# Kernel optimization log

Hardware: AMD Instinct MI355X
Metric: run time of the kernel (lower is better)

Reference implementation:

```python
import jax, jax.numpy as jnp
import numpy as np

V, E, D, T, B = 32000, 512, 512, 512, 32
PAD = 3

def layer_norm(x, g, b, eps=1e-5):
    m = jnp.mean(x, axis=-1, keepdims=True)
    v = jnp.mean((x - m) ** 2, axis=-1, keepdims=True)
    return (x - m) * jax.lax.rsqrt(v + eps) * g + b

def sru_direction(U, v, b, reverse):
    # U: (T, B, 4D) -> splits: x_tilde, f-gate pre-act, r-gate pre-act, highway input
    x_t, uf, ur, xp = jnp.split(U, 4, axis=-1)
    def step(c, inp):
        xt, uft, urt, xpt = inp
        f = jax.nn.sigmoid(uft + v[0] * c + b[0])
        r = jax.nn.sigmoid(urt + v[1] * c + b[1])
        c_new = f * c + (1.0 - f) * xt
        h = r * c_new + (1.0 - r) * xpt
        return c_new, h
    c0 = jnp.zeros((U.shape[1], v.shape[1]), U.dtype)  # (B, D)
    c_last, hs = jax.lax.scan(step, c0, (x_t, uf, ur, xp), reverse=reverse)
    return hs, c_last

def setup_inputs() -> dict:
    key = jax.random.key(0)
    ks = jax.random.split(key, 8)
    def rn(k, shp, sc=0.05):
        return jax.random.normal(k, shp, jnp.float32) * sc
    return {
        "src": jax.random.randint(ks[0], (T, B), 0, V),
        "emb": rn(ks[1], (V, E), 0.1),
        "ln_g": jnp.ones((E,), jnp.float32),
        "ln_b": jnp.zeros((E,), jnp.float32),
        "W0": rn(ks[2], (E, 4 * D)),
        "W1": rn(ks[3], (E, 4 * D)),
        "v0": rn(ks[4], (2, D), 0.5),
        "v1": rn(ks[5], (2, D), 0.5),
        "b0": jnp.zeros((2, D), jnp.float32),
        "b1": jnp.zeros((2, D), jnp.float32),
        "W_out": rn(ks[6], (D, 2 * D)),
        "b_out": jnp.zeros((D,), jnp.float32),
    }

def reference(src, emb, ln_g, ln_b, W0, W1, v0, v1, b0, b1, W_out, b_out):
    table = emb.at[PAD].set(0.0)          # padding_idx row is zero
    x = table[src]                         # (T, B, E); dropout p=0 -> identity
    xn = layer_norm(x, ln_g, ln_b)         # SRU layer_norm=True: LN on cell input
    h0, c0 = sru_direction(jnp.einsum('tbe,ef->tbf', xn, W0), v0, b0, False)
    h1, c1 = sru_direction(jnp.einsum('tbe,ef->tbf', xn, W1), v1, b1, True)
    outputs = jnp.concatenate([h0, h1], axis=-1)        # (T, B, 2D)
    hidden = jnp.concatenate([c0, c1], axis=-1)[None]   # (1, B, 2D)
    out = jnp.tanh(jnp.einsum('tbh,dh->tbd', outputs, W_out) + b_out)
    return out, hidden
```

## Files before the change

### kernel.cpp

```cpp
#include <hip/hip_runtime.h>
#include <cstdint>
#include <cstddef>

#define T_DIM 512
#define B_DIM 32
#define E_DIM 512
#define D_DIM 512
#define PAD_IDX 3
#define M_ROWS (T_DIM * B_DIM)
#define PF 32

typedef __attribute__((ext_vector_type(8))) __bf16 bf16x8;
typedef __attribute__((ext_vector_type(4))) float  f32x4;

__device__ __forceinline__ unsigned short f2bf(float x) {
    union { float f; uint32_t u; } v; v.f = x;
    uint32_t u = v.u;
    uint32_t r = (u + 0x7FFFu + ((u >> 16) & 1u)) >> 16;
    return (unsigned short)r;
}
__device__ __forceinline__ float bf2f(unsigned short h) {
    union { float f; uint32_t u; } v; v.u = ((uint32_t)h) << 16;
    return v.f;
}
__device__ __forceinline__ float fast_sigmoid(float z) {
    return __builtin_amdgcn_rcpf(1.f + __expf(-z));
}
__device__ __forceinline__ float fast_tanh(float x) {
    return 1.f - 2.f * __builtin_amdgcn_rcpf(__expf(2.f * x) + 1.f);
}

__global__ __launch_bounds__(256) void prep_kernel(
    const int* __restrict__ src, const float* __restrict__ emb,
    const float* __restrict__ g, const float* __restrict__ bb,
    const float* __restrict__ W0, const float* __restrict__ W1,
    const float* __restrict__ b0, const float* __restrict__ b1,
    const float* __restrict__ W_out,
    unsigned short* __restrict__ xn, unsigned short* __restrict__ Wt,
    unsigned short* __restrict__ Wob, float* __restrict__ bias)
{
    __shared__ float tile[64][65];
    const int bx = blockIdx.x;
    if (bx < 4096) {
        int wave = threadIdx.x >> 6;
        int lane = threadIdx.x & 63;
        int row  = bx * 4 + wave;
        int tok  = src[row];
        float x[8];
        if (tok == PAD_IDX) {
            #pragma unroll
            for (int j = 0; j < 8; j++) x[j] = 0.f;
        } else {
            const float* er = emb + (size_t)tok * E_DIM + lane * 8;
            f32x4 a0 = *(const f32x4*)(er);
            f32x4 a1 = *(const f32x4*)(er + 4);
            #pragma unroll
            for (int j = 0; j < 4; j++) { x[j] = a0[j]; x[4 + j] = a1[j]; }
        }
        float s = 0.f, sq = 0.f;
        #pragma unroll
        for (int j = 0; j < 8; j++) { s += x[j]; sq += x[j] * x[j]; }
        #pragma unroll
        for (int off = 32; off >= 1; off >>= 1) {
            s  += __shfl_xor(s,  off, 64);
            sq += __shfl_xor(sq, off, 64);
        }
        float mean = s * (1.f / 512.f);
        float var  = sq * (1.f / 512.f) - mean * mean;
        float rs   = rsqrtf(var + 1e-5f);
        f32x4 g0 = *(const f32x4*)(g + lane * 8);
        f32x4 g1 = *(const f32x4*)(g + lane * 8 + 4);
        f32x4 c0 = *(const f32x4*)(bb + lane * 8);
        f32x4 c1 = *(const f32x4*)(bb + lane * 8 + 4);
        unsigned short o[8];
        #pragma unroll
        for (int j = 0; j < 4; j++) {
            o[j]     = f2bf((x[j]     - mean) * rs * g0[j] + c0[j]);
            o[4 + j] = f2bf((x[4 + j] - mean) * rs * g1[j] + c1[j]);
        }
        uint4 pk;
        pk.x = (uint32_t)o[0] | ((uint32_t)o[1] << 16);
        pk.y = (uint32_t)o[2] | ((uint32_t)o[3] << 16);
        pk.z = (uint32_t)o[4] | ((uint32_t)o[5] << 16);
        pk.w = (uint32_t)o[6] | ((uint32_t)o[7] << 16);
        *(uint4*)(xn + (size_t)row * E_DIM + lane * 8) = pk;
    } else if (bx < 4608) {
        int bxx = bx - 4096;
        int k0  = (bxx & 7) * 64;
        int n0g = (bxx >> 3) * 64;
        int dir = n0g >> 11;
        const float* W = dir ? W1 : W0;
        int d0 = (n0g & 2047) >> 2;
        int tx = threadIdx.x & 63;
        int ty = threadIdx.x >> 6;
        int scol = ((tx >> 4) << 9) + d0 + (tx & 15);
        for (int r = ty; r < 64; r += 4)
            tile[r][tx] = W[(size_t)(k0 + r) * 2048 + scol];
        __syncthreads();
        for (int r2 = ty; r2 < 64; r2 += 4) {
            int j = ((r2 & 3) << 4) | (r2 >> 2);
            Wt[(size_t)(n0g + r2) * 512 + k0 + tx] = f2bf(tile[tx][j]);
        }
    } else if (bx < 5120) {
        int i = ((bx - 4608) * 256 + threadIdx.x) * 4;
        f32x4 v = *(const f32x4*)(W_out + i);
        uint2 pk;
        pk.x = (uint32_t)f2bf(v[0]) | ((uint32_t)f2bf(v[1]) << 16);
        pk.y = (uint32_t)f2bf(v[2]) | ((uint32_t)f2bf(v[3]) << 16);
        *(uint2*)(Wob + i) = pk;
    } else {
        int n = (bx - 5120) * 256 + threadIdx.x;
        int dir = n >> 11, gg = n & 3, d = (n & 2047) >> 2;
        const float* bp = dir ? b1 : b0;
        float v = (gg == 1) ? bp[d] : ((gg == 2) ? bp[512 + d] : 0.f);
        bias[n] = v;
    }
}

template<int KD, int NMT, int NNT, int GM, int GN, int EPI>
__global__ __launch_bounds__(512, 4) void gemm_pipe_kernel(
    const unsigned short* __restrict__ A,
    const unsigned short* __restrict__ Bt,
    void* __restrict__ Cout,
    const float* __restrict__ bias,
    int ldc)
{
    constexpr int BM = 128, BN = 256;
    constexpr int MR = 4, NR = 4;
    constexpr int NKT = KD / 32;
    constexpr int RA  = BM / 128;
    constexpr int RB  = BN / 128;
    constexpr int LPT = RA + RB;
    constexpr int ASZ = BM * 32;
    constexpr int BSZ = BN * 32;
    __shared__ unsigned short smem[3 * (ASZ + BSZ)];

    const int tid = threadIdx.x;
    const int w   = tid >> 6;
    const int l   = tid & 63;

    constexpr int PER_G = GM * GN;
    constexpr int NGC   = NNT / GN;
    const int bid = blockIdx.x;
    const int c   = bid & 7;
    const int idx = bid >> 3;
    const int gi  = idx / PER_G;
    const int wi  = idx % PER_G;
    const int gg  = c + 8 * gi;
    const int mt  = (gg / NGC) * GM + wi / GN;
    const int nt  = (gg % NGC) * GN + wi % GN;

    const int wm = w >> 2, wn = w & 3;

    const unsigned short* Ab = A  + (size_t)mt * BM * KD;
    const unsigned short* Bb = Bt + (size_t)nt * BN * KD;

    const int srow = w * 16 + (l >> 2);
    const int scol = ((l & 3) ^ ((l >> 3) & 3)) * 8;

    auto stage = [&](int t, int slot) {
        const unsigned short* Ag = Ab + t * 32;
        const unsigned short* Bg = Bb + t * 32;
        unsigned short* As = smem + slot * (ASZ + BSZ);
        unsigned short* Bs = As + ASZ;
        #pragma unroll
        for (int r = 0; r < RA; r++)
            __builtin_amdgcn_global_load_lds(
                (const __attribute__((address_space(1))) void*)(Ag + (size_t)(r * 128 + srow) * KD + scol),
                (__attribute__((address_space(3))) void*)(As + (r * 128 + w * 16) * 32),
                16, 0, 0);
        #pragma unroll
        for (int r = 0; r < RB; r++)
            __builtin_amdgcn_global_load_lds(
                (const __attribute__((address_space(1))) void*)(Bg + (size_t)(r * 128 + srow) * KD + scol),
                (__attribute__((address_space(3))) void*)(Bs + (r * 128 + w * 16) * 32),
                16, 0, 0);
    };

    f32x4 acc[MR][NR];
    #pragma unroll
    for (int m = 0; m < MR; m++)
        #pragma unroll
        for (int n = 0; n < NR; n++)
            acc[m][n] = (f32x4){0.f, 0.f, 0.f, 0.f};

    stage(0, 0); stage(1, 1);

    const int li   = l & 15;
    const int cg   = l >> 4;
    const int rswz = (cg ^ ((li >> 1) & 3)) * 8;

    #pragma unroll
    for (int t = 0; t < NKT; t++) {
        if (t + 1 < NKT)
            asm volatile("s_waitcnt vmcnt(%0) lgkmcnt(0)" :: "n"(LPT) : "memory");
        else
            asm volatile("s_waitcnt vmcnt(0) lgkmcnt(0)" ::: "memory");
        __builtin_amdgcn_s_barrier();
        if (t + 2 < NKT) stage(t + 2, (t + 2) % 3);

        const unsigned short* As = smem + (t % 3) * (ASZ + BSZ);
        const unsigned short* Bs = As + ASZ;
        bf16x8 af[MR], bfv[NR];
        #pragma unroll
        for (int m = 0; m < MR; m++) {
            int row = wm * 64 + m * 16 + li;
            af[m] = *(const bf16x8*)(As + row * 32 + rswz);
        }
        #pragma unroll
        for (int n = 0; n < NR; n++) {
            int row = wn * 64 + n * 16 + li;
            bfv[n] = *(const bf16x8*)(Bs + row * 32 + rswz);
        }
        __builtin_amdgcn_s_setprio(1);
        #pragma unroll
        for (int m = 0; m < MR; m++)
            #pragma unroll
            for (int n = 0; n < NR; n++)
                acc[m][n] = __builtin_amdgcn_mfma_f32_16x16x32_bf16(
                    af[m], bfv[n], acc[m][n], 0, 0, 0);
        __builtin_amdgcn_s_setprio(0);
    }

    const int colb = nt * BN + wn * 64;
    const int rowb = mt * BM + wm * 64;
    #pragma unroll
    for (int m = 0; m < MR; m++) {
        #pragma unroll
        for (int n = 0; n < NR; n++) {
            int col  = colb + n * 16 + li;
            int row0 = rowb + m * 16 + cg * 4;
            float bi = bias[col];
            if (EPI == 0) {
                unsigned short* C = (unsigned short*)Cout;
                #pragma unroll
                for (int j = 0; j < 4; j++)
                    C[(size_t)(row0 + j) * ldc + col] = f2bf(acc[m][n][j] + bi);
            } else {
                float* C = (float*)Cout;
                #pragma unroll
                for (int j = 0; j < 4; j++)
                    C[(size_t)(row0 + j) * ldc + col] = fast_tanh(acc[m][n][j] + bi);
            }
        }
    }
}

template<int KD, int NMT, int NNT, int GM, int GN, int EPI>
__global__ __launch_bounds__(256, 3) void gemm_ring3_kernel(
    const unsigned short* __restrict__ A,
    const unsigned short* __restrict__ Bt,
    void* __restrict__ Cout,
    const float* __restrict__ bias,
    int ldc)
{
    constexpr int NKT = KD / 32;
    constexpr int LPT = 4;
    constexpr int SLOT = 8192;
    __shared__ unsigned short smem[3 * SLOT];

    const int tid = threadIdx.x;
    const int w   = tid >> 6;
    const int l   = tid & 63;

    constexpr int PER_G = GM * GN;
    constexpr int NGC   = NNT / GN;
    const int bid = blockIdx.x;
    const int c   = bid & 7;
    const int idx = bid >> 3;
    const int gi  = idx / PER_G;
    const int wi  = idx % PER_G;
    const int gg  = c + 8 * gi;
    const int mt  = (gg / NGC) * GM + wi / GN;
    const int nt  = (gg % NGC) * GN + wi % GN;

    const int wm = w >> 1, wn = w & 1;

    const unsigned short* Ab = A  + (size_t)mt * 128 * KD;
    const unsigned short* Bb = Bt + (size_t)nt * 128 * KD;

    const int s_colx = (((l & 3) ^ ((l >> 3) & 3)) * 8);

    auto stage = [&](int t, int slot) {
        const unsigned short* Ag = Ab + t * 32 + s_colx;
        const unsigned short* Bg = Bb + t * 32 + s_colx;
        unsigned short* As = smem + slot * SLOT;
        unsigned short* Bs = As + 4096;
        #pragma unroll
        for (int r = 0; r < 2; r++) {
            int grow = r * 64 + w * 16 + (l >> 2);
            __builtin_amdgcn_global_load_lds(
                (const __attribute__((address_space(1))) void*)(Ag + (size_t)grow * KD),
                (__attribute__((address_space(3))) void*)(As + r * 2048 + w * 512),
                16, 0, 0);
            __builtin_amdgcn_global_load_lds(
                (const __attribute__((address_space(1))) void*)(Bg + (size_t)grow * KD),
                (__attribute__((address_space(3))) void*)(Bs + r * 2048 + w * 512),
                16, 0, 0);
        }
    };

    f32x4 acc[4][4];
    #pragma unroll
    for (int m = 0; m < 4; m++)
        #pragma unroll
        for (int n = 0; n < 4; n++)
            acc[m][n] = (f32x4){0.f, 0.f, 0.f, 0.f};

    stage(0, 0); stage(1, 1);

    const int li   = l & 15;
    const int cg   = l >> 4;
    const int rswz = (cg ^ ((li >> 1) & 3)) * 8;

    #pragma unroll
    for (int t = 0; t < NKT; t++) {
        if (t + 1 < NKT)
            asm volatile("s_waitcnt vmcnt(%0) lgkmcnt(0)" :: "n"(LPT) : "memory");
        else
            asm volatile("s_waitcnt vmcnt(0) lgkmcnt(0)" ::: "memory");
        __builtin_amdgcn_s_barrier();
        if (t + 2 < NKT) stage(t + 2, (t + 2) % 3);

        const unsigned short* As = smem + (t % 3) * SLOT;
        const unsigned short* Bs = As + 4096;
        bf16x8 af[4], bfv[4];
        #pragma unroll
        for (int m = 0; m < 4; m++) {
            int row = wm * 64 + m * 16 + li;
            af[m] = *(const bf16x8*)(As + row * 32 + rswz);
        }
        #pragma unroll
        for (int n = 0; n < 4; n++) {
            int row = wn * 64 + n * 16 + li;
            bfv[n] = *(const bf16x8*)(Bs + row * 32 + rswz);
        }
        __builtin_amdgcn_s_setprio(1);
        #pragma unroll
        for (int m = 0; m < 4; m++)
            #pragma unroll
            for (int n = 0; n < 4; n++)
                acc[m][n] = __builtin_amdgcn_mfma_f32_16x16x32_bf16(
                    af[m], bfv[n], acc[m][n], 0, 0, 0);
        __builtin_amdgcn_s_setprio(0);
    }

    const int colb = nt * 128 + wn * 64;
    const int rowb = mt * 128 + wm * 64;
    #pragma unroll
    for (int m = 0; m < 4; m++) {
        #pragma unroll
        for (int n = 0; n < 4; n++) {
            int col  = colb + n * 16 + li;
            int row0 = rowb + m * 16 + cg * 4;
            float bi = bias[col];
            if (EPI == 0) {
                unsigned short* C = (unsigned short*)Cout;
                #pragma unroll
                for (int j = 0; j < 4; j++)
                    C[(size_t)(row0 + j) * ldc + col] = f2bf(acc[m][n][j] + bi);
            } else {
                float* C = (float*)Cout;
                #pragma unroll
                for (int j = 0; j < 4; j++)
                    C[(size_t)(row0 + j) * ldc + col] = fast_tanh(acc[m][n][j] + bi);
            }
        }
    }
}

__global__ __launch_bounds__(64) void sru_scan_kernel(
    const unsigned short* __restrict__ U,
    const float* __restrict__ v0, const float* __restrict__ v1,
    unsigned short* __restrict__ h,
    float* __restrict__ hidden)
{
    int id  = blockIdx.x * 64 + threadIdx.x;
    int dir = id >> 14;
    int rem = id & 16383;
    int b   = rem >> 9;
    int d   = rem & 511;
    const float* v = dir ? v1 : v0;
    float vf = v[d], vr = v[D_DIM + d];

    int row0  = (dir ? (T_DIM - 1) * B_DIM : 0) + b;
    long step = (long)(dir ? -B_DIM : B_DIM) * 1024;

    const ushort4* lp = (const ushort4*)U + (size_t)row0 * 1024 + dir * 512 + d;
    unsigned short* hp = h + (size_t)row0 * 1024 + dir * 512 + d;

    ushort4 buf[PF];
    #pragma unroll
    for (int p = 0; p < PF; p++) { buf[p] = *lp; lp += step; }

    float c = 0.f;
    for (int tb = 0; tb < T_DIM - PF; tb += PF) {
        #pragma unroll
        for (int p = 0; p < PF; p++) {
            ushort4 q = buf[p];
            buf[p] = *lp; lp += step;
            float x  = bf2f(q.x);
            float uf = bf2f(q.y);
            float ur = bf2f(q.z);
            float xp = bf2f(q.w);
            float f = fast_sigmoid(__fmaf_rn(vf, c, uf));
            float r = fast_sigmoid(__fmaf_rn(vr, c, ur));
            c = __fmaf_rn(f, c - x, x);
            float hv = __fmaf_rn(r, c - xp, xp);
            *hp = f2bf(hv); hp += step;
        }
    }
    #pragma unroll
    for (int p = 0; p < PF; p++) {
        ushort4 q = buf[p];
        float x  = bf2f(q.x);
        float uf = bf2f(q.y);
        float ur = bf2f(q.z);
        float xp = bf2f(q.w);
        float f = fast_sigmoid(__fmaf_rn(vf, c, uf));
        float r = fast_sigmoid(__fmaf_rn(vr, c, ur));
        c = __fmaf_rn(f, c - x, x);
        float hv = __fmaf_rn(r, c - xp, xp);
        *hp = f2bf(hv); hp += step;
    }
    hidden[b * 1024 + dir * 512 + d] = c;
}

extern "C" void kernel_launch(void* const* d_in, const int* in_sizes, int n_in,
                              void* d_out, int out_size, void* d_ws, size_t ws_size,
                              hipStream_t stream)
{
    const int*   src   = (const int*)  d_in[0];
    const float* emb   = (const float*)d_in[1];
    const float* ln_g  = (const float*)d_in[2];
    const float* ln_b  = (const float*)d_in[3];
    const float* W0    = (const float*)d_in[4];
    const float* W1    = (const float*)d_in[5];
    const float* v0    = (const float*)d_in[6];
    const float* v1    = (const float*)d_in[7];
    const float* b0    = (const float*)d_in[8];
    const float* b1    = (const float*)d_in[9];
    const float* W_out = (const float*)d_in[10];
    const float* b_out = (const float*)d_in[11];

    unsigned short* Wt  = (unsigned short*)d_ws;
    unsigned short* Wob = Wt  + (size_t)4096 * 512;
    unsigned short* xn  = Wob + (size_t)512 * 1024;
    unsigned short* U   = xn  + (size_t)M_ROWS * 512;
    unsigned short* h   = U   + (size_t)M_ROWS * 4096;
    float*          bias4096 = (float*)(h + (size_t)M_ROWS * 1024);

    float* out    = (float*)d_out;
    float* hidden = out + (size_t)M_ROWS * D_DIM;
    (void)out;

    prep_kernel<<<5136, 256, 0, stream>>>(src, emb, ln_g, ln_b, W0, W1,
                                          b0, b1, W_out, xn, Wt, Wob, bias4096);

    gemm_pipe_kernel<512, 128, 16, 8, 4, 0>
        <<<2048, 512, 0, stream>>>(xn, Wt, (void*)U, bias4096, 4096);

    sru_scan_kernel<<<512, 64, 0, stream>>>(U, v0, v1, h, hidden);

    gemm_ring3_kernel<1024, 128, 4, 8, 2, 1>
        <<<512, 256, 0, stream>>>(h, Wob, (void*)d_out, b_out, 512);
}
```

Measured before the change: 154.1 us.

## Load B operand straight into registers for the input GEMM and reuse pipe kernel for output GEMM

Adds a GEMM variant for the large U projection in which each wave loads its B (weight) fragments directly from global memory into a double-buffered register array. Only the A tile is staged through LDS with a three-slot ring. This shrinks LDS use and the B-side LDS traffic, at the cost of more VGPRs and uncoalesced 16-byte global loads. The output projection switches from the 256-thread ring3 kernel to the 512-thread, 128x256-tile pipe kernel with 256 blocks, and the ring3 kernel is removed.

```diff
diff --git a/kernel.cpp b/kernel.cpp
--- a/kernel.cpp
+++ b/kernel.cpp
@@ -117,6 +117,118 @@
     }
 }
 
+template<int KD, int NMT, int NNT, int GM, int GN>
+__global__ __launch_bounds__(512, 4) void gemm_breg_kernel(
+    const unsigned short* __restrict__ A,
+    const unsigned short* __restrict__ Bt,
+    unsigned short* __restrict__ C,
+    const float* __restrict__ bias,
+    int ldc)
+{
+    constexpr int NKT = KD / 32;
+    constexpr int ASZ = 128 * 32;
+    __shared__ unsigned short smem[3 * ASZ];
+
+    const int tid = threadIdx.x;
+    const int w   = tid >> 6;
+    const int l   = tid & 63;
+
+    constexpr int PER_G = GM * GN;
+    constexpr int NGC   = NNT / GN;
+    const int bid = blockIdx.x;
+    const int c   = bid & 7;
+    const int idx = bid >> 3;
+    const int gi  = idx / PER_G;
+    const int wi  = idx % PER_G;
+    const int gg  = c + 8 * gi;
+    const int mt  = (gg / NGC) * GM + wi / GN;
+    const int nt  = (gg % NGC) * GN + wi % GN;
+
+    const int wm = w >> 2, wn = w & 3;
+    const int li = l & 15;
+    const int cg = l >> 4;
+
+    const unsigned short* Ab = A + (size_t)mt * 128 * KD;
+    const unsigned short* bp = Bt + (size_t)(nt * 256 + wn * 64 + li) * KD + cg * 8;
+
+    const int srow = w * 16 + (l >> 2);
+    const int scol = ((l & 3) ^ ((l >> 3) & 3)) * 8;
+
+    auto stageA = [&](int t, int slot) {
+        __builtin_amdgcn_global_load_lds(
+            (const __attribute__((address_space(1))) void*)(Ab + (size_t)srow * KD + t * 32 + scol),
+            (__attribute__((address_space(3))) void*)(smem + slot * ASZ + (w * 16) * 32),
+            16, 0, 0);
+    };
+
+    f32x4 acc[4][4];
+    #pragma unroll
+    for (int m = 0; m < 4; m++)
+        #pragma unroll
+        for (int n = 0; n < 4; n++)
+            acc[m][n] = (f32x4){0.f, 0.f, 0.f, 0.f};
+
+    bf16x8 bB[2][4];
+
+    stageA(0, 0);
+    #pragma unroll
+    for (int n = 0; n < 4; n++)
+        bB[0][n] = *(const bf16x8*)(bp + (size_t)n * 16 * KD);
+    stageA(1, 1);
+    #pragma unroll
+    for (int n = 0; n < 4; n++)
+        bB[1][n] = *(const bf16x8*)(bp + (size_t)n * 16 * KD + 32);
+
+    const int rswz = (cg ^ ((li >> 1) & 3)) * 8;
+
+    #pragma unroll
+    for (int t = 0; t < NKT; t++) {
+        if (t + 1 < NKT)
+            asm volatile("s_waitcnt vmcnt(5) lgkmcnt(0)" ::: "memory");
+        else
+            asm volatile("s_waitcnt vmcnt(0) lgkmcnt(0)" ::: "memory");
+        __builtin_amdgcn_s_barrier();
+        if (t + 2 < NKT) stageA(t + 2, (t + 2) % 3);
+
+        const unsigned short* As = smem + (t % 3) * ASZ;
+        bf16x8 af[4];
+        #pragma unroll
+        for (int m = 0; m < 4; m++) {
+            int row = wm * 64 + m * 16 + li;
+            af[m] = *(const bf16x8*)(As + row * 32 + rswz);
+        }
+        __builtin_amdgcn_s_setprio(1);
+        #pragma unroll
+        for (int m = 0; m < 4; m++)
+            #pragma unroll
+            for (int n = 0; n < 4; n++)
+                acc[m][n] = __builtin_amdgcn_mfma_f32_16x16x32_bf16(
+                    af[m], bB[t % 2][n], acc[m][n], 0, 0, 0);
+        __builtin_amdgcn_s_setprio(0);
+
+        if (t + 2 < NKT) {
+            #pragma unroll
+            for (int n = 0; n < 4; n++)
+                bB[t % 2][n] = *(const bf16x8*)(bp + (size_t)n * 16 * KD + (t + 2) * 32);
+        }
+    }
+
+    const int colb = nt * 256 + wn * 64;
+    const int rowb = mt * 128 + wm * 64;
+    #pragma unroll
+    for (int m = 0; m < 4; m++) {
+        #pragma unroll
+        for (int n = 0; n < 4; n++) {
+            int col  = colb + n * 16 + li;
+            int row0 = rowb + m * 16 + cg * 4;
+            float bi = bias[col];
+            #pragma unroll
+            for (int j = 0; j < 4; j++)
+                C[(size_t)(row0 + j) * ldc + col] = f2bf(acc[m][n][j] + bi);
+        }
+    }
+}
+
 template<int KD, int NMT, int NNT, int GM, int GN, int EPI>
 __global__ __launch_bounds__(512, 4) void gemm_pipe_kernel(
     const unsigned short* __restrict__ A,
@@ -246,129 +358,6 @@
     }
 }
 
-template<int KD, int NMT, int NNT, int GM, int GN, int EPI>
-__global__ __launch_bounds__(256, 3) void gemm_ring3_kernel(
-    const unsigned short* __restrict__ A,
-    const unsigned short* __restrict__ Bt,
-    void* __restrict__ Cout,
-    const float* __restrict__ bias,
-    int ldc)
-{
-    constexpr int NKT = KD / 32;
-    constexpr int LPT = 4;
-    constexpr int SLOT = 8192;
-    __shared__ unsigned short smem[3 * SLOT];
-
-    const int tid = threadIdx.x;
-    const int w   = tid >> 6;
-    const int l   = tid & 63;
-
-    constexpr int PER_G = GM * GN;
-    constexpr int NGC   = NNT / GN;
-    const int bid = blockIdx.x;
-    const int c   = bid & 7;
-    const int idx = bid >> 3;
-    const int gi  = idx / PER_G;
-    const int wi  = idx % PER_G;
-    const int gg  = c + 8 * gi;
-    const int mt  = (gg / NGC) * GM + wi / GN;
-    const int nt  = (gg % NGC) * GN + wi % GN;
-
-    const int wm = w >> 1, wn = w & 1;
-
-    const unsigned short* Ab = A  + (size_t)mt * 128 * KD;
-    const unsigned short* Bb = Bt + (size_t)nt * 128 * KD;
-
-    const int s_colx = (((l & 3) ^ ((l >> 3) & 3)) * 8);
-
-    auto stage = [&](int t, int slot) {
-        const unsigned short* Ag = Ab + t * 32 + s_colx;
-        const unsigned short* Bg = Bb + t * 32 + s_colx;
-        unsigned short* As = smem + slot * SLOT;
-        unsigned short* Bs = As + 4096;
-        #pragma unroll
-        for (int r = 0; r < 2; r++) {
-            int grow = r * 64 + w * 16 + (l >> 2);
-            __builtin_amdgcn_global_load_lds(
-                (const __attribute__((address_space(1))) void*)(Ag + (size_t)grow * KD),
-                (__attribute__((address_space(3))) void*)(As + r * 2048 + w * 512),
-                16, 0, 0);
-            __builtin_amdgcn_global_load_lds(
-                (const __attribute__((address_space(1))) void*)(Bg + (size_t)grow * KD),
-                (__attribute__((address_space(3))) void*)(Bs + r * 2048 + w * 512),
-                16, 0, 0);
-        }
-    };
-
-    f32x4 acc[4][4];
-    #pragma unroll
-    for (int m = 0; m < 4; m++)
-        #pragma unroll
-        for (int n = 0; n < 4; n++)
-            acc[m][n] = (f32x4){0.f, 0.f, 0.f, 0.f};
-
-    stage(0, 0); stage(1, 1);
-
-    const int li   = l & 15;
-    const int cg   = l >> 4;
-    const int rswz = (cg ^ ((li >> 1) & 3)) * 8;
-
-    #pragma unroll
-    for (int t = 0; t < NKT; t++) {
-        if (t + 1 < NKT)
-            asm volatile("s_waitcnt vmcnt(%0) lgkmcnt(0)" :: "n"(LPT) : "memory");
-        else
-            asm volatile("s_waitcnt vmcnt(0) lgkmcnt(0)" ::: "memory");
-        __builtin_amdgcn_s_barrier();
-        if (t + 2 < NKT) stage(t + 2, (t + 2) % 3);
-
-        const unsigned short* As = smem + (t % 3) * SLOT;
-        const unsigned short* Bs = As + 4096;
-        bf16x8 af[4], bfv[4];
-        #pragma unroll
-        for (int m = 0; m < 4; m++) {
-            int row = wm * 64 + m * 16 + li;
-            af[m] = *(const bf16x8*)(As + row * 32 + rswz);
-        }
-        #pragma unroll
-        for (int n = 0; n < 4; n++) {
-            int row = wn * 64 + n * 16 + li;
-            bfv[n] = *(const bf16x8*)(Bs + row * 32 + rswz);
-        }
-        __builtin_amdgcn_s_setprio(1);
-        #pragma unroll
-        for (int m = 0; m < 4; m++)
-            #pragma unroll
-            for (int n = 0; n < 4; n++)
-                acc[m][n] = __builtin_amdgcn_mfma_f32_16x16x32_bf16(
-                    af[m], bfv[n], acc[m][n], 0, 0, 0);
-        __builtin_amdgcn_s_setprio(0);
-    }
-
-    const int colb = nt * 128 + wn * 64;
-    const int rowb = mt * 128 + wm * 64;
-    #pragma unroll
-    for (int m = 0; m < 4; m++) {
-        #pragma unroll
-        for (int n = 0; n < 4; n++) {
-            int col  = colb + n * 16 + li;
-            int row0 = rowb + m * 16 + cg * 4;
-            float bi = bias[col];
-            if (EPI == 0) {
-                unsigned short* C = (unsigned short*)Cout;
-                #pragma unroll
-                for (int j = 0; j < 4; j++)
-                    C[(size_t)(row0 + j) * ldc + col] = f2bf(acc[m][n][j] + bi);
-            } else {
-                float* C = (float*)Cout;
-                #pragma unroll
-                for (int j = 0; j < 4; j++)
-                    C[(size_t)(row0 + j) * ldc + col] = fast_tanh(acc[m][n][j] + bi);
-            }
-        }
-    }
-}
-
 __global__ __launch_bounds__(64) void sru_scan_kernel(
     const unsigned short* __restrict__ U,
     const float* __restrict__ v0, const float* __restrict__ v1,
@@ -457,11 +446,11 @@
     prep_kernel<<<5136, 256, 0, stream>>>(src, emb, ln_g, ln_b, W0, W1,
                                           b0, b1, W_out, xn, Wt, Wob, bias4096);
 
-    gemm_pipe_kernel<512, 128, 16, 8, 4, 0>
-        <<<2048, 512, 0, stream>>>(xn, Wt, (void*)U, bias4096, 4096);
+    gemm_breg_kernel<512, 128, 16, 8, 4>
+        <<<2048, 512, 0, stream>>>(xn, Wt, U, bias4096, 4096);
 
     sru_scan_kernel<<<512, 64, 0, stream>>>(U, v0, v1, h, hidden);
 
-    gemm_ring3_kernel<1024, 128, 4, 8, 2, 1>
-        <<<512, 256, 0, stream>>>(h, Wob, (void*)d_out, b_out, 512);
-}
+    gemm_pipe_kernel<1024, 128, 2, 8, 2, 1>
+        <<<256, 512, 0, stream>>>(h, Wob, (void*)d_out, b_out, 512);
+}
```

New measurement: 213.0 us. 38.2% more time.
